# Optimization experiments

Measured on AMD Instinct MI355X. Metric: run time of the kernel, lower is better.

## Reference

```python
import jax, jax.numpy as jnp
import numpy as np

EPS = 1e-8


def setup_inputs() -> dict:
    key = jax.random.key(0)
    k1, k2 = jax.random.split(key)
    latent = jax.random.normal(k1, (16, 192, 64, 64), dtype=jnp.float32)
    codebook = jax.random.normal(k2, (1024, 192), dtype=jnp.float32)
    # codebook rows are unit-normalized at init in the original module
    codebook = codebook / jnp.linalg.norm(codebook, axis=-1, keepdims=True)
    return {"latent": latent, "codebook": codebook}


def reference(latent, codebook):
    b, c, h, w = latent.shape
    # [B,C,H,W] -> [N, C]
    x = jnp.transpose(latent, (0, 2, 3, 1)).reshape(-1, c)
    x = x / (jnp.linalg.norm(x, axis=-1, keepdims=True) + EPS)
    x2 = jnp.sum(x * x, axis=-1, keepdims=True)            # [N,1]
    c2 = jnp.sum(codebook * codebook, axis=-1)             # [K]
    dist_sq = x2 - 2.0 * jnp.einsum('nd,kd->nk', x, codebook) + c2[None, :]
    indices = jnp.argmin(dist_sq, axis=-1)                 # [N]
    quantized_flat = codebook[indices]                     # [N,C] gather
    quantized = jnp.transpose(quantized_flat.reshape(b, h, w, c), (0, 3, 1, 2))
    return quantized, indices.reshape(b, h, w)
```

## Files before the change

kernel.cpp:

```cpp
#include <hip/hip_runtime.h>


#define NPTS   65536
#define DIMS   192
#define KCB    1024
#define HW     4096
#define QELEMS 12582912

typedef __attribute__((ext_vector_type(8))) _Float16 f16x8;
typedef __attribute__((ext_vector_type(4))) _Float16 f16x4;
typedef __attribute__((ext_vector_type(4))) float f32x4;


__device__ __forceinline__ void async_load16(const void* g, void* l) {
    __builtin_amdgcn_global_load_lds(
        (const __attribute__((address_space(1))) unsigned int*)g,
        (__attribute__((address_space(3))) unsigned int*)l, 16, 0, 0);
}

__device__ __forceinline__ void top3_ins(unsigned& b, unsigned& s, unsigned& t,
                                         unsigned p) {
    unsigned m1 = min(b, p);
    unsigned m2 = min(s, p);
    b = max(b, p);
    s = max(s, m1);
    t = max(t, m2);
}

__global__ __launch_bounds__(256) void k_prep(const float* __restrict__ cbk,
                                              _Float16* __restrict__ Bpf,
                                              float* __restrict__ cbkT,
                                              float* __restrict__ c2) {
    __shared__ float q[16 * 193];
    const int tid = threadIdx.x;
    const int k0 = blockIdx.x * 16;
    const int lane = tid & 63;
    const int grp = tid >> 6;
    for (int r = grp; r < 16; r += 4) {
        const float* row = cbk + (size_t)(k0 + r) * DIMS;
        for (int c = lane; c < DIMS; c += 64) q[r * 193 + c] = row[c];
    }
    __syncthreads();
    {
        const int kl = tid & 15, dg = tid >> 4;
        for (int d = dg; d < DIMS; d += 16)
            cbkT[(size_t)d * KCB + k0 + kl] = q[kl * 193 + d];
    }
    for (int r = grp; r < 16; r += 4)
        for (int c = lane; c < DIMS; c += 64)
            Bpf[((size_t)(c >> 6) * KCB + k0 + r) * 64 + (c & 63)] =
                (_Float16)q[r * 193 + c];
    if (tid < 16) {
        float s = 0.f;
        #pragma unroll 4
        for (int c = 0; c < DIMS; ++c) {
            float v = q[tid * 193 + c];
            s = fmaf(v, v, s);
        }
        c2[k0 + tid] = s;
    }
}

__global__ __launch_bounds__(256, 2) void k_gemm_f(const float* __restrict__ latent,
                                                   const _Float16* __restrict__ Bpf,
                                                   const float* __restrict__ cbkT,
                                                   const float* __restrict__ c2,
                                                   const float* __restrict__ cbk,
                                                   float* __restrict__ out_q,
                                                   float* __restrict__ idxf) {
    __shared__ __align__(16) _Float16 As[128 * 200];
    __shared__ __align__(16) _Float16 Bs[2][4096];
    __shared__ float nrm_s[128];
    __shared__ uint4 t2buf[256];
    __shared__ int sidx[128];
    __shared__ int slist_pair[128];
    __shared__ int slist_full[128];
    __shared__ int scnt_pair, scnt_full;
    __shared__ float part8[8][32];
    __shared__ float inv8[8];
    __shared__ unsigned long long best8[8];

    const int tid = threadIdx.x;
    const int wave = tid >> 6;
    const int lane = tid & 63;
    const int quad = lane >> 4;
    const int l15 = lane & 15;
    const int wm = (wave >> 1) * 64;
    const int wn = (wave & 1) * 64;
    const int n0 = blockIdx.x * 128;
    const int bB = n0 >> 12;
    const int hw0 = n0 & 4095;
    const size_t latb = (size_t)bB * DIMS * HW;

    {
        float* part = (float*)&Bs[0][0];
        const float* lat = latent + latb + hw0;
        const int p = tid & 127, ch = tid >> 7;
        float ss = 0.f;
        #pragma unroll 4
        for (int i = 0; i < 24; ++i) {
            int c0 = i * 8 + ch * 4;
            float v0 = lat[(size_t)(c0 + 0) * HW + p];
            float v1 = lat[(size_t)(c0 + 1) * HW + p];
            float v2 = lat[(size_t)(c0 + 2) * HW + p];
            float v3 = lat[(size_t)(c0 + 3) * HW + p];
            ss = fmaf(v0, v0, fmaf(v1, v1, fmaf(v2, v2, fmaf(v3, v3, ss))));
            f16x4 h = { (_Float16)v0, (_Float16)v1, (_Float16)v2, (_Float16)v3 };
            *(f16x4*)&As[p * 200 + c0] = h;
        }
        part[ch * 128 + p] = ss;
        __syncthreads();
        if (tid < 128)
            nrm_s[tid] = sqrtf(part[tid] + part[128 + tid]);
        if (tid == 0) { scnt_pair = 0; scnt_full = 0; }
        __syncthreads();
    }

    const int sk0 = tid >> 2,        sj0 = (tid & 3) ^ ((sk0 >> 1) & 3);
    const int sk1 = (tid + 256) >> 2, sj1 = ((tid + 256) & 3) ^ ((sk1 >> 1) & 3);

    async_load16(Bpf + ((size_t)sk0) * 64 + sj0 * 8, &Bs[0][tid * 8]);
    async_load16(Bpf + ((size_t)sk1) * 64 + sj1 * 8, &Bs[0][(tid + 256) * 8]);

    unsigned rb[16], rs[16], rt[16];
    #pragma unroll
    for (int i = 0; i < 16; ++i) { rb[i] = 0u; rs[i] = 0u; rt[i] = 0u; }

    int nb_s = 0, h_s = 1;

    for (int nb = 0; nb < 8; ++nb) {
        f32x4 acc[4][4];
        #pragma unroll
        for (int mt = 0; mt < 4; ++mt)
            #pragma unroll
            for (int nt = 0; nt < 4; ++nt)
                #pragma unroll
                for (int r = 0; r < 4; ++r) acc[mt][nt][r] = 0.f;

        #pragma unroll
        for (int h = 0; h < 6; ++h) {
            const int ph = nb * 6 + h;
            asm volatile("s_waitcnt vmcnt(0)" ::: "memory");
            __syncthreads();
            if (ph < 47) {
                const size_t gb = ((size_t)(h_s >> 1) * KCB + nb_s * 128) * 64
                                  + (h_s & 1) * 32;
                async_load16(Bpf + gb + (size_t)sk0 * 64 + sj0 * 8,
                             &Bs[(ph + 1) & 1][tid * 8]);
                async_load16(Bpf + gb + (size_t)sk1 * 64 + sj1 * 8,
                             &Bs[(ph + 1) & 1][(tid + 256) * 8]);
                if (++h_s == 6) { h_s = 0; ++nb_s; }
            }
            const int g = h >> 1, s = h & 1;
            f16x8 af[4], bfr[4];
            #pragma unroll
            for (int mt = 0; mt < 4; ++mt) {
                int m = wm + mt * 16 + l15;
                af[mt] = *(const f16x8*)&As[m * 200 + g * 64 + s * 32 + quad * 8];
            }
            #pragma unroll
            for (int nt = 0; nt < 4; ++nt) {
                int n = wn + nt * 16 + l15;
                bfr[nt] = *(const f16x8*)&Bs[ph & 1][n * 32 + (quad ^ ((n >> 1) & 3)) * 8];
            }
            #pragma unroll
            for (int mt = 0; mt < 4; ++mt)
                #pragma unroll
                for (int nt = 0; nt < 4; ++nt)
                    acc[mt][nt] = __builtin_amdgcn_mfma_f32_16x16x32_f16(
                        af[mt], bfr[nt], acc[mt][nt], 0, 0, 0);
        }

        int kbase = nb * 128 + wn;
        #pragma unroll
        for (int mt = 0; mt < 4; ++mt) {
            #pragma unroll
            for (int r = 0; r < 4; ++r) {
                const int i = mt * 4 + r;
                #pragma unroll
                for (int nt = 0; nt < 4; ++nt) {
                    unsigned pv = ((unsigned)fmaf(acc[mt][nt][r], 65536.f, 2097152.f) << 10)
                                  | (unsigned)(kbase + nt * 16 + l15);
                    top3_ins(rb[i], rs[i], rt[i], pv);
                }
            }
        }
    }

    __syncthreads();
    #pragma unroll
    for (int i = 0; i < 16; ++i) {
        unsigned b = rb[i], s = rs[i], t = rt[i];
        #pragma unroll
        for (int off = 1; off < 16; off <<= 1) {
            unsigned ob = __shfl_xor(b, off, 64);
            unsigned os = __shfl_xor(s, off, 64);
            unsigned ot = __shfl_xor(t, off, 64);
            top3_ins(b, s, t, ob);
            top3_ins(b, s, t, os);
            top3_ins(b, s, t, ot);
        }
        if (l15 == 0) {
            int mt = i >> 2, r = i & 3;
            int mloc = wm + mt * 16 + quad * 4 + r;
            t2buf[mloc * 2 + (wave & 1)] = make_uint4(b, s, t, 0u);
        }
    }
    __syncthreads();
    if (tid < 128) {
        uint4 x = t2buf[tid * 2];
        uint4 y = t2buf[tid * 2 + 1];
        unsigned b = x.x, s = x.y, t = x.z;
        top3_ins(b, s, t, y.x);
        top3_ins(b, s, t, y.y);
        top3_ins(b, s, t, y.z);
        sidx[tid] = (int)(b & 1023u);
        unsigned q1 = b >> 10, q2 = s >> 10, q3 = t >> 10;
        unsigned Mq = (unsigned)fmaf(152.0f, nrm_s[tid], 4.0f);
        if (q1 - q3 < Mq) {
            int pos = atomicAdd(&scnt_full, 1);
            slist_full[pos] = tid;
        } else if (q1 - q2 < Mq) {
            int pos = atomicAdd(&scnt_pair, 1);
            slist_pair[pos] = tid | ((int)(b & 1023u) << 7)
                                  | ((int)(s & 1023u) << 17);
        }
    }
    __syncthreads();
    const int nfull = scnt_full;
    const int npair = scnt_pair;

    {
        float* xsf = (float*)As;
        const float4* ct = (const float4*)cbkT;
        const int j8 = tid >> 5, dl = tid & 31;
        for (int base = 0; base < nfull; base += 8) {
            const bool valid = (base + j8) < nfull;
            const int ploc = valid ? slist_full[base + j8] : 0;
            float ss = 0.f;
            if (valid) {
                #pragma unroll
                for (int i = 0; i < 6; ++i) {
                    int d = dl + i * 32;
                    float v = latent[latb + (size_t)d * HW + hw0 + ploc];
                    xsf[j8 * 200 + d] = v;
                    ss = fmaf(v, v, ss);
                }
            }
            part8[j8][dl] = ss;
            if (tid < 8) best8[tid] = ~0ull;
            __syncthreads();
            if (tid < 8) {
                float s = 0.f;
                #pragma unroll
                for (int i = 0; i < 32; ++i) s += part8[tid][i];
                inv8[tid] = 1.0f / (sqrtf(s) + 1e-8f);
            }
            __syncthreads();
            float4 a[8];
            #pragma unroll
            for (int p = 0; p < 8; ++p) a[p] = make_float4(0.f, 0.f, 0.f, 0.f);
            for (int d = 0; d < DIMS; d += 4) {
                float4 cv0 = ct[(size_t)(d + 0) * 256 + tid];
                float4 cv1 = ct[(size_t)(d + 1) * 256 + tid];
                float4 cv2 = ct[(size_t)(d + 2) * 256 + tid];
                float4 cv3 = ct[(size_t)(d + 3) * 256 + tid];
                #pragma unroll
                for (int p = 0; p < 8; ++p) {
                    float4 xv = *(const float4*)&xsf[p * 200 + d];
                    a[p].x = fmaf(xv.x, cv0.x, a[p].x); a[p].y = fmaf(xv.x, cv0.y, a[p].y);
                    a[p].z = fmaf(xv.x, cv0.z, a[p].z); a[p].w = fmaf(xv.x, cv0.w, a[p].w);
                    a[p].x = fmaf(xv.y, cv1.x, a[p].x); a[p].y = fmaf(xv.y, cv1.y, a[p].y);
                    a[p].z = fmaf(xv.y, cv1.z, a[p].z); a[p].w = fmaf(xv.y, cv1.w, a[p].w);
                    a[p].x = fmaf(xv.z, cv2.x, a[p].x); a[p].y = fmaf(xv.z, cv2.y, a[p].y);
                    a[p].z = fmaf(xv.z, cv2.z, a[p].z); a[p].w = fmaf(xv.z, cv2.w, a[p].w);
                    a[p].x = fmaf(xv.w, cv3.x, a[p].x); a[p].y = fmaf(xv.w, cv3.y, a[p].y);
                    a[p].z = fmaf(xv.w, cv3.z, a[p].z); a[p].w = fmaf(xv.w, cv3.w, a[p].w);
                }
            }
            #pragma unroll
            for (int p = 0; p < 8; ++p) {
                float inv = inv8[p];
                float dot4[4] = {a[p].x, a[p].y, a[p].z, a[p].w};
                unsigned long long loc = ~0ull;
                #pragma unroll
                for (int e = 0; e < 4; ++e) {
                    int k = 4 * tid + e;
                    float dist = c2[k] - 2.f * inv * dot4[e];
                    unsigned ub = __float_as_uint(dist);
                    ub ^= (ub >> 31) ? 0xFFFFFFFFu : 0x80000000u;
                    unsigned long long pk =
                        ((unsigned long long)ub << 32) | (unsigned)k;
                    loc = loc < pk ? loc : pk;
                }
                #pragma unroll
                for (int off = 1; off < 64; off <<= 1) {
                    unsigned long long o = __shfl_xor(loc, off, 64);
                    loc = loc < o ? loc : o;
                }
                if ((tid & 63) == 0) atomicMin(&best8[p], loc);
            }
            __syncthreads();
            if (valid && dl == 0)
                sidx[ploc] = (int)(best8[j8] & 0xFFFFFFFFull);
            __syncthreads();
        }
    }

    for (int i = tid; i < npair; i += 256) {
        int pk = slist_pair[i];
        int ploc = pk & 127;
        int k1 = (pk >> 7) & 1023;
        int k2 = (pk >> 17) & 1023;
        const float* xr = latent + latb + hw0 + ploc;
        const float* c1 = cbk + (size_t)k1 * DIMS;
        const float* c2r = cbk + (size_t)k2 * DIMS;
        float a1 = 0.f, a2 = 0.f;
        float pp[16];
        #pragma unroll
        for (int e = 0; e < 16; ++e) pp[e] = 0.f;
        for (int d0 = 0; d0 < DIMS; d0 += 16) {
            #pragma unroll
            for (int e = 0; e < 16; ++e) {
                int d = d0 + e;
                float xv = xr[(size_t)d * HW];
                a1 = fmaf(xv, c1[d], a1);
                a2 = fmaf(xv, c2r[d], a2);
                pp[e] = fmaf(xv, xv, pp[e]);
            }
        }
        float ss = 0.f;
        #pragma unroll
        for (int e = 0; e < 16; ++e) ss += pp[e];
        float inv = 1.0f / (sqrtf(ss) + 1e-8f);
        float d1 = c2[k1] - 2.f * inv * a1;
        float d2 = c2[k2] - 2.f * inv * a2;
        unsigned u1 = __float_as_uint(d1);
        u1 ^= (u1 >> 31) ? 0xFFFFFFFFu : 0x80000000u;
        unsigned u2 = __float_as_uint(d2);
        u2 ^= (u2 >> 31) ? 0xFFFFFFFFu : 0x80000000u;
        unsigned long long p1 = ((unsigned long long)u1 << 32) | (unsigned)k1;
        unsigned long long p2 = ((unsigned long long)u2 << 32) | (unsigned)k2;
        sidx[ploc] = (int)((p1 < p2 ? p1 : p2) & 1023ull);
    }
    __syncthreads();

    if (tid < 128) idxf[n0 + tid] = (float)sidx[tid];
    __syncthreads();

    float* q = (float*)As;
    for (int chk = 0; chk < 4; ++chk) {
        int p0 = chk * 32;
        for (int r = wave; r < 32; r += 4) {
            const float* row = cbk + (size_t)sidx[p0 + r] * DIMS;
            for (int c = lane; c < DIMS; c += 64) q[r * 193 + c] = row[c];
        }
        __syncthreads();
        float* ob = out_q + latb + hw0 + p0;
        #pragma unroll
        for (int i = 0; i < 24; ++i) {
            int u = i * 256 + tid;
            int c = u >> 5, p = u & 31;
            ob[(size_t)c * HW + p] = q[p * 193 + c];
        }
        __syncthreads();
    }
}

__global__ __launch_bounds__(256) void k_norms_fb(const float* __restrict__ latent,
                                                  float* __restrict__ inv_norm) {
    __shared__ float red[256];
    const int tid = threadIdx.x;
    const int n0 = blockIdx.x * 128;
    const int nl = tid & 127;
    const int half = tid >> 7;
    const int b = n0 >> 12;
    const int hw = (n0 & 4095) + nl;
    const float* base = latent + (size_t)b * DIMS * HW + hw;
    float ssq = 0.f;
    for (int c = half; c < DIMS; c += 2) {
        float v = base[(size_t)c * HW];
        ssq = fmaf(v, v, ssq);
    }
    red[tid] = ssq;
    __syncthreads();
    if (half == 0) {
        float s = red[tid] + red[tid + 128];
        inv_norm[n0 + nl] = 1.0f / (sqrtf(s) + 1e-8f);
    }
}

__global__ __launch_bounds__(256) void k_c2_fb(const float* __restrict__ cbk,
                                               float* __restrict__ c2) {
    int k = blockIdx.x * 256 + threadIdx.x;
    if (k >= KCB) return;
    const float4* row = (const float4*)(cbk + (size_t)k * DIMS);
    float s = 0.f;
    #pragma unroll
    for (int i = 0; i < DIMS / 4; ++i) {
        float4 v = row[i];
        s += v.x * v.x + v.y * v.y + v.z * v.z + v.w * v.w;
    }
    c2[k] = s;
}

#define LDX  132
__global__ __launch_bounds__(256) void k_dist_fb(const float* __restrict__ latent,
                                                 const float* __restrict__ cbk,
                                                 const float* __restrict__ inv_norm,
                                                 const float* __restrict__ c2,
                                                 int* __restrict__ idx_out,
                                                 float* __restrict__ idxf_out) {
    __shared__ __align__(16) float xsm[64 * LDX];
    __shared__ __align__(16) float csm[64 * LDX];
    __shared__ unsigned long long red[128];
    const int tid = threadIdx.x;
    const int n0 = blockIdx.x * 128;
    const int b = n0 >> 12;
    const int hw0 = n0 & 4095;
    const int kt = tid & 15;
    const int mt = tid >> 4;
    const float* lat_base = latent + (size_t)b * DIMS * HW + hw0;
    float inv[8];
    #pragma unroll
    for (int i = 0; i < 8; ++i) inv[i] = inv_norm[n0 + mt * 8 + i];
    float best[8];
    int bidx[8];
    #pragma unroll
    for (int i = 0; i < 8; ++i) { best[i] = 3.4e38f; bidx[i] = 0; }
    const int nl = tid & 127;
    const int cp = tid >> 7;
    for (int k0 = 0; k0 < KCB; k0 += 128) {
        float acc[8][8];
        #pragma unroll
        for (int i = 0; i < 8; ++i)
            #pragma unroll
            for (int j = 0; j < 8; ++j) acc[i][j] = 0.f;
        for (int d0 = 0; d0 < DIMS; d0 += 64) {
            __syncthreads();
            for (int cc = cp; cc < 64; cc += 2)
                xsm[cc * LDX + nl] = lat_base[(size_t)(d0 + cc) * HW + nl];
            #pragma unroll
            for (int i = 0; i < 8; ++i) {
                int f4 = tid + 256 * i;
                int kk = f4 >> 4;
                int dq = f4 & 15;
                float4 v = *(const float4*)(cbk + (size_t)(k0 + kk) * DIMS + d0 + dq * 4);
                csm[(dq * 4 + 0) * LDX + kk] = v.x;
                csm[(dq * 4 + 1) * LDX + kk] = v.y;
                csm[(dq * 4 + 2) * LDX + kk] = v.z;
                csm[(dq * 4 + 3) * LDX + kk] = v.w;
            }
            __syncthreads();
            for (int d = 0; d < 64; ++d) {
                const float* xr = &xsm[d * LDX + mt * 8];
                const float* cr = &csm[d * LDX + kt * 8];
                float x8[8], c8[8];
                *(float4*)&x8[0] = *(const float4*)&xr[0];
                *(float4*)&x8[4] = *(const float4*)&xr[4];
                *(float4*)&c8[0] = *(const float4*)&cr[0];
                *(float4*)&c8[4] = *(const float4*)&cr[4];
                #pragma unroll
                for (int i = 0; i < 8; ++i)
                    #pragma unroll
                    for (int j = 0; j < 8; ++j)
                        acc[i][j] = fmaf(x8[i], c8[j], acc[i][j]);
            }
        }
        float cc2[8];
        #pragma unroll
        for (int j = 0; j < 8; ++j) cc2[j] = c2[k0 + kt * 8 + j];
        #pragma unroll
        for (int i = 0; i < 8; ++i)
            #pragma unroll
            for (int j = 0; j < 8; ++j) {
                float t = inv[i] * acc[i][j];
                float dist = fmaf(-2.f, t, cc2[j]);
                int kidx = k0 + kt * 8 + j;
                if (dist < best[i]) { best[i] = dist; bidx[i] = kidx; }
            }
    }
    if (tid < 128) red[tid] = ~0ull;
    __syncthreads();
    #pragma unroll
    for (int i = 0; i < 8; ++i) {
        unsigned long long p =
            ((unsigned long long)__float_as_uint(best[i]) << 32) | (unsigned)bidx[i];
        atomicMin(&red[mt * 8 + i], p);
    }
    __syncthreads();
    if (tid < 128) {
        int k = (int)(red[tid] & 0xFFFFFFFFu);
        idx_out[n0 + tid] = k;
        idxf_out[n0 + tid] = (float)k;
    }
}

__global__ __launch_bounds__(256) void k_gather(const float* __restrict__ cbk,
                                                const int* __restrict__ idx,
                                                float* __restrict__ out) {
    __shared__ float q[64 * 193];
    __shared__ int sidx[64];
    const int tid = threadIdx.x;
    const int n0 = blockIdx.x * 64;
    const int b = n0 >> 12;
    const int hw0 = n0 & 4095;
    const int lane = tid & 63;
    const int grp = tid >> 6;

    if (tid < 64) sidx[tid] = idx[n0 + tid];
    __syncthreads();
    for (int r = grp; r < 64; r += 4) {
        const float* row = cbk + (size_t)sidx[r] * DIMS;
        for (int c = lane; c < DIMS; c += 64) q[r * 193 + c] = row[c];
    }
    __syncthreads();
    float* obase = out + (size_t)b * DIMS * HW + hw0;
    for (int c = grp; c < DIMS; c += 4) {
        obase[(size_t)c * HW + lane] = q[lane * 193 + c];
    }
}

extern "C" void kernel_launch(void* const* d_in, const int* in_sizes, int n_in,
                              void* d_out, int out_size, void* d_ws, size_t ws_size,
                              hipStream_t stream) {
    const float* latent = (const float*)d_in[0];
    const float* cbk = (const float*)d_in[1];
    float* out = (float*)d_out;
    float* out_q = out;
    float* out_idx = out + QELEMS;

    if (ws_size >= 2u * 1024u * 1024u) {
        char* w = (char*)d_ws;
        _Float16* Bpf = (_Float16*)w;
        float* cbkT = (float*)(w + 393216);
        float* c2 = (float*)(w + 1179648);

        k_prep<<<KCB / 16, 256, 0, stream>>>(cbk, Bpf, cbkT, c2);
        k_gemm_f<<<512, 256, 0, stream>>>(latent, Bpf, cbkT, c2, cbk,
                                          out_q, out_idx);
    } else {
        float* inv_norm = (float*)d_ws;
        float* c2 = inv_norm + NPTS;
        int* idx = (int*)(c2 + KCB);
        k_norms_fb<<<NPTS / 128, 256, 0, stream>>>(latent, inv_norm);
        k_c2_fb<<<4, 256, 0, stream>>>(cbk, c2);
        k_dist_fb<<<NPTS / 128, 256, 0, stream>>>(latent, cbk, inv_norm, c2, idx, out_idx);
        k_gather<<<NPTS / 64, 256, 0, stream>>>(cbk, idx, out_q);
    }
}
```

Baseline: 194.9 us.

## Triple-buffer codebook tiles with deeper async prefetch and overlay epilogue smem

Codebook B tiles go from double to triple buffering. The async loads are now issued two phases ahead, and each phase waits with vmcnt(2) instead of vmcnt(0), so global-to-LDS latency overlaps more of the MFMA work. The first two tiles are prefetched before the latent load and normalization, overlapping that setup with codebook fetches. To keep LDS usage, and so the 2-blocks-per-CU occupancy, roughly unchanged, the epilogue scratch arrays are overlaid onto a dead region of As. This depends on careful offsets and on correct barrier ordering.

```diff
diff --git a/kernel.cpp b/kernel.cpp
--- a/kernel.cpp
+++ b/kernel.cpp
@@ -69,16 +69,19 @@
                                                    float* __restrict__ out_q,
                                                    float* __restrict__ idxf) {
     __shared__ __align__(16) _Float16 As[128 * 200];
-    __shared__ __align__(16) _Float16 Bs[2][4096];
+    __shared__ __align__(16) _Float16 Bs[3][4096];
     __shared__ float nrm_s[128];
-    __shared__ uint4 t2buf[256];
-    __shared__ int sidx[128];
-    __shared__ int slist_pair[128];
-    __shared__ int slist_full[128];
-    __shared__ int scnt_pair, scnt_full;
-    __shared__ float part8[8][32];
-    __shared__ float inv8[8];
-    __shared__ unsigned long long best8[8];
+    __shared__ float part0[256];
+
+    char* ovl = (char*)As + 32768;
+    uint4* t2buf = (uint4*)ovl;
+    int* sidx = (int*)(ovl + 4096);
+    int* slist_pair = (int*)(ovl + 4608);
+    int* slist_full = (int*)(ovl + 5120);
+    int* scnts = (int*)(ovl + 5632);
+    float* part8 = (float*)(ovl + 5696);
+    float* inv8 = (float*)(ovl + 6720);
+    unsigned long long* best8 = (unsigned long long*)(ovl + 6784);
 
     const int tid = threadIdx.x;
     const int wave = tid >> 6;
@@ -92,8 +95,15 @@
     const int hw0 = n0 & 4095;
     const size_t latb = (size_t)bB * DIMS * HW;
 
+    const int sk0 = tid >> 2,         sj0 = (tid & 3) ^ ((sk0 >> 1) & 3);
+    const int sk1 = (tid + 256) >> 2, sj1 = ((tid + 256) & 3) ^ ((sk1 >> 1) & 3);
+
+    async_load16(Bpf + (size_t)sk0 * 64 + sj0 * 8, &Bs[0][tid * 8]);
+    async_load16(Bpf + (size_t)sk1 * 64 + sj1 * 8, &Bs[0][(tid + 256) * 8]);
+    async_load16(Bpf + (size_t)sk0 * 64 + sj0 * 8 + 32, &Bs[1][tid * 8]);
+    async_load16(Bpf + (size_t)sk1 * 64 + sj1 * 8 + 32, &Bs[1][(tid + 256) * 8]);
+
     {
-        float* part = (float*)&Bs[0][0];
         const float* lat = latent + latb + hw0;
         const int p = tid & 127, ch = tid >> 7;
         float ss = 0.f;
@@ -108,25 +118,19 @@
             f16x4 h = { (_Float16)v0, (_Float16)v1, (_Float16)v2, (_Float16)v3 };
             *(f16x4*)&As[p * 200 + c0] = h;
         }
-        part[ch * 128 + p] = ss;
+        part0[ch * 128 + p] = ss;
         __syncthreads();
         if (tid < 128)
-            nrm_s[tid] = sqrtf(part[tid] + part[128 + tid]);
-        if (tid == 0) { scnt_pair = 0; scnt_full = 0; }
+            nrm_s[tid] = sqrtf(part0[tid] + part0[128 + tid]);
         __syncthreads();
     }
-
-    const int sk0 = tid >> 2,        sj0 = (tid & 3) ^ ((sk0 >> 1) & 3);
-    const int sk1 = (tid + 256) >> 2, sj1 = ((tid + 256) & 3) ^ ((sk1 >> 1) & 3);
-
-    async_load16(Bpf + ((size_t)sk0) * 64 + sj0 * 8, &Bs[0][tid * 8]);
-    async_load16(Bpf + ((size_t)sk1) * 64 + sj1 * 8, &Bs[0][(tid + 256) * 8]);
 
     unsigned rb[16], rs[16], rt[16];
     #pragma unroll
     for (int i = 0; i < 16; ++i) { rb[i] = 0u; rs[i] = 0u; rt[i] = 0u; }
 
-    int nb_s = 0, h_s = 1;
+    int bc = 0;
+    int nb_s = 0, h_s = 2;
 
     for (int nb = 0; nb < 8; ++nb) {
         f32x4 acc[4][4];
@@ -139,16 +143,21 @@
 
         #pragma unroll
         for (int h = 0; h < 6; ++h) {
-            const int ph = nb * 6 + h;
-            asm volatile("s_waitcnt vmcnt(0)" ::: "memory");
-            __syncthreads();
-            if (ph < 47) {
+            if (nb == 7 && h == 5) {
+                asm volatile("s_waitcnt vmcnt(0)" ::: "memory");
+            } else {
+                asm volatile("s_waitcnt vmcnt(2)" ::: "memory");
+            }
+            __builtin_amdgcn_s_barrier();
+            asm volatile("" ::: "memory");
+            if (!(nb == 7 && h >= 4)) {
+                const int bt = (bc >= 1) ? bc - 1 : bc + 2;
                 const size_t gb = ((size_t)(h_s >> 1) * KCB + nb_s * 128) * 64
                                   + (h_s & 1) * 32;
                 async_load16(Bpf + gb + (size_t)sk0 * 64 + sj0 * 8,
-                             &Bs[(ph + 1) & 1][tid * 8]);
+                             &Bs[bt][tid * 8]);
                 async_load16(Bpf + gb + (size_t)sk1 * 64 + sj1 * 8,
-                             &Bs[(ph + 1) & 1][(tid + 256) * 8]);
+                             &Bs[bt][(tid + 256) * 8]);
                 if (++h_s == 6) { h_s = 0; ++nb_s; }
             }
             const int g = h >> 1, s = h & 1;
@@ -161,7 +170,7 @@
             #pragma unroll
             for (int nt = 0; nt < 4; ++nt) {
                 int n = wn + nt * 16 + l15;
-                bfr[nt] = *(const f16x8*)&Bs[ph & 1][n * 32 + (quad ^ ((n >> 1) & 3)) * 8];
+                bfr[nt] = *(const f16x8*)&Bs[bc][n * 32 + (quad ^ ((n >> 1) & 3)) * 8];
             }
             #pragma unroll
             for (int mt = 0; mt < 4; ++mt)
@@ -169,6 +178,7 @@
                 for (int nt = 0; nt < 4; ++nt)
                     acc[mt][nt] = __builtin_amdgcn_mfma_f32_16x16x32_f16(
                         af[mt], bfr[nt], acc[mt][nt], 0, 0, 0);
+            bc = (bc == 2) ? 0 : bc + 1;
         }
 
         int kbase = nb * 128 + wn;
@@ -188,6 +198,7 @@
     }
 
     __syncthreads();
+    if (tid == 0) { scnts[0] = 0; scnts[1] = 0; }
     #pragma unroll
     for (int i = 0; i < 16; ++i) {
         unsigned b = rb[i], s = rs[i], t = rt[i];
@@ -218,17 +229,17 @@
         unsigned q1 = b >> 10, q2 = s >> 10, q3 = t >> 10;
         unsigned Mq = (unsigned)fmaf(152.0f, nrm_s[tid], 4.0f);
         if (q1 - q3 < Mq) {
-            int pos = atomicAdd(&scnt_full, 1);
+            int pos = atomicAdd(&scnts[1], 1);
             slist_full[pos] = tid;
         } else if (q1 - q2 < Mq) {
-            int pos = atomicAdd(&scnt_pair, 1);
+            int pos = atomicAdd(&scnts[0], 1);
             slist_pair[pos] = tid | ((int)(b & 1023u) << 7)
                                   | ((int)(s & 1023u) << 17);
         }
     }
     __syncthreads();
-    const int nfull = scnt_full;
-    const int npair = scnt_pair;
+    const int nfull = scnts[1];
+    const int npair = scnts[0];
 
     {
         float* xsf = (float*)As;
@@ -247,13 +258,13 @@
                     ss = fmaf(v, v, ss);
                 }
             }
-            part8[j8][dl] = ss;
+            part8[j8 * 32 + dl] = ss;
             if (tid < 8) best8[tid] = ~0ull;
             __syncthreads();
             if (tid < 8) {
                 float s = 0.f;
                 #pragma unroll
-                for (int i = 0; i < 32; ++i) s += part8[tid][i];
+                for (int i = 0; i < 32; ++i) s += part8[tid * 32 + i];
                 inv8[tid] = 1.0f / (sqrtf(s) + 1e-8f);
             }
             __syncthreads();
```

Result: no change. 191.6 us (-1.7%).

## Halve points per block, overlay scratch LDS on B buffer, raise occupancy

Applied to the files above, without the earlier changes.

The fused GEMM/argmin kernel now handles 64 points per block instead of 128, launching 1024 blocks, and each wave computes 32 rows instead of 64. The post-GEMM scratch arrays (top-3 buffer, index lists, refinement buffers) are aliased onto the B double buffer, and the first B tile prefetch is issued before the latent load, shrinking LDS so launch bounds can request 3 blocks per CU. The aim is better latency hiding and an earlier start on the codebook fetch, at the cost of reloading the codebook tiles twice as often across blocks and doing less MFMA work per B fragment loaded.

```diff
diff --git a/kernel.cpp b/kernel.cpp
--- a/kernel.cpp
+++ b/kernel.cpp
@@ -61,45 +61,54 @@
     }
 }
 
-__global__ __launch_bounds__(256, 2) void k_gemm_f(const float* __restrict__ latent,
+__global__ __launch_bounds__(256, 3) void k_gemm_f(const float* __restrict__ latent,
                                                    const _Float16* __restrict__ Bpf,
                                                    const float* __restrict__ cbkT,
                                                    const float* __restrict__ c2,
                                                    const float* __restrict__ cbk,
                                                    float* __restrict__ out_q,
                                                    float* __restrict__ idxf) {
-    __shared__ __align__(16) _Float16 As[128 * 200];
+    __shared__ __align__(16) _Float16 As[64 * 200];
     __shared__ __align__(16) _Float16 Bs[2][4096];
-    __shared__ float nrm_s[128];
-    __shared__ uint4 t2buf[256];
-    __shared__ int sidx[128];
-    __shared__ int slist_pair[128];
-    __shared__ int slist_full[128];
-    __shared__ int scnt_pair, scnt_full;
-    __shared__ float part8[8][32];
-    __shared__ float inv8[8];
-    __shared__ unsigned long long best8[8];
+    __shared__ float nrm_s[64];
+    __shared__ float part0[256];
+
+    char* ovl = (char*)Bs;
+    uint4* t2buf = (uint4*)ovl;
+    int* sidx = (int*)(ovl + 2048);
+    int* slist_pair = (int*)(ovl + 2304);
+    int* slist_full = (int*)(ovl + 2560);
+    int* scnts = (int*)(ovl + 2816);
+    float* part8 = (float*)(ovl + 2824);
+    float* inv8 = (float*)(ovl + 3848);
+    unsigned long long* best8 = (unsigned long long*)(ovl + 3880);
+    float* xsf = (float*)(ovl + 8192);
 
     const int tid = threadIdx.x;
     const int wave = tid >> 6;
     const int lane = tid & 63;
     const int quad = lane >> 4;
     const int l15 = lane & 15;
-    const int wm = (wave >> 1) * 64;
+    const int wm = (wave >> 1) * 32;
     const int wn = (wave & 1) * 64;
-    const int n0 = blockIdx.x * 128;
+    const int n0 = blockIdx.x * 64;
     const int bB = n0 >> 12;
     const int hw0 = n0 & 4095;
     const size_t latb = (size_t)bB * DIMS * HW;
 
+    const int sk0 = tid >> 2,         sj0 = (tid & 3) ^ ((sk0 >> 1) & 3);
+    const int sk1 = (tid + 256) >> 2, sj1 = ((tid + 256) & 3) ^ ((sk1 >> 1) & 3);
+
+    async_load16(Bpf + (size_t)sk0 * 64 + sj0 * 8, &Bs[0][tid * 8]);
+    async_load16(Bpf + (size_t)sk1 * 64 + sj1 * 8, &Bs[0][(tid + 256) * 8]);
+
     {
-        float* part = (float*)&Bs[0][0];
         const float* lat = latent + latb + hw0;
-        const int p = tid & 127, ch = tid >> 7;
+        const int p = tid & 63, ch = tid >> 6;
         float ss = 0.f;
         #pragma unroll 4
-        for (int i = 0; i < 24; ++i) {
-            int c0 = i * 8 + ch * 4;
+        for (int i = 0; i < 12; ++i) {
+            int c0 = i * 16 + ch * 4;
             float v0 = lat[(size_t)(c0 + 0) * HW + p];
             float v1 = lat[(size_t)(c0 + 1) * HW + p];
             float v2 = lat[(size_t)(c0 + 2) * HW + p];
@@ -108,30 +117,24 @@
             f16x4 h = { (_Float16)v0, (_Float16)v1, (_Float16)v2, (_Float16)v3 };
             *(f16x4*)&As[p * 200 + c0] = h;
         }
-        part[ch * 128 + p] = ss;
+        part0[ch * 64 + p] = ss;
         __syncthreads();
-        if (tid < 128)
-            nrm_s[tid] = sqrtf(part[tid] + part[128 + tid]);
-        if (tid == 0) { scnt_pair = 0; scnt_full = 0; }
+        if (tid < 64)
+            nrm_s[tid] = sqrtf(part0[tid] + part0[64 + tid] +
+                               part0[128 + tid] + part0[192 + tid]);
         __syncthreads();
     }
 
-    const int sk0 = tid >> 2,        sj0 = (tid & 3) ^ ((sk0 >> 1) & 3);
-    const int sk1 = (tid + 256) >> 2, sj1 = ((tid + 256) & 3) ^ ((sk1 >> 1) & 3);
-
-    async_load16(Bpf + ((size_t)sk0) * 64 + sj0 * 8, &Bs[0][tid * 8]);
-    async_load16(Bpf + ((size_t)sk1) * 64 + sj1 * 8, &Bs[0][(tid + 256) * 8]);
-
-    unsigned rb[16], rs[16], rt[16];
+    unsigned rb[8], rs[8], rt[8];
     #pragma unroll
-    for (int i = 0; i < 16; ++i) { rb[i] = 0u; rs[i] = 0u; rt[i] = 0u; }
+    for (int i = 0; i < 8; ++i) { rb[i] = 0u; rs[i] = 0u; rt[i] = 0u; }
 
     int nb_s = 0, h_s = 1;
 
     for (int nb = 0; nb < 8; ++nb) {
-        f32x4 acc[4][4];
-        #pragma unroll
-        for (int mt = 0; mt < 4; ++mt)
+        f32x4 acc[2][4];
+        #pragma unroll
+        for (int mt = 0; mt < 2; ++mt)
             #pragma unroll
             for (int nt = 0; nt < 4; ++nt)
                 #pragma unroll
@@ -152,9 +155,9 @@
                 if (++h_s == 6) { h_s = 0; ++nb_s; }
             }
             const int g = h >> 1, s = h & 1;
-            f16x8 af[4], bfr[4];
-            #pragma unroll
-            for (int mt = 0; mt < 4; ++mt) {
+            f16x8 af[2], bfr[4];
+            #pragma unroll
+            for (int mt = 0; mt < 2; ++mt) {
                 int m = wm + mt * 16 + l15;
                 af[mt] = *(const f16x8*)&As[m * 200 + g * 64 + s * 32 + quad * 8];
             }
@@ -164,7 +167,7 @@
                 bfr[nt] = *(const f16x8*)&Bs[ph & 1][n * 32 + (quad ^ ((n >> 1) & 3)) * 8];
             }
             #pragma unroll
-            for (int mt = 0; mt < 4; ++mt)
+            for (int mt = 0; mt < 2; ++mt)
                 #pragma unroll
                 for (int nt = 0; nt < 4; ++nt)
                     acc[mt][nt] = __builtin_amdgcn_mfma_f32_16x16x32_f16(
@@ -173,7 +176,7 @@
 
         int kbase = nb * 128 + wn;
         #pragma unroll
-        for (int mt = 0; mt < 4; ++mt) {
+        for (int mt = 0; mt < 2; ++mt) {
             #pragma unroll
             for (int r = 0; r < 4; ++r) {
                 const int i = mt * 4 + r;
@@ -188,8 +191,9 @@
     }
 
     __syncthreads();
+    if (tid == 0) { scnts[0] = 0; scnts[1] = 0; }
     #pragma unroll
-    for (int i = 0; i < 16; ++i) {
+    for (int i = 0; i < 8; ++i) {
         unsigned b = rb[i], s = rs[i], t = rt[i];
         #pragma unroll
         for (int off = 1; off < 16; off <<= 1) {
@@ -207,7 +211,7 @@
         }
     }
     __syncthreads();
-    if (tid < 128) {
+    if (tid < 64) {
         uint4 x = t2buf[tid * 2];
         uint4 y = t2buf[tid * 2 + 1];
         unsigned b = x.x, s = x.y, t = x.z;
@@ -218,20 +222,19 @@
         unsigned q1 = b >> 10, q2 = s >> 10, q3 = t >> 10;
         unsigned Mq = (unsigned)fmaf(152.0f, nrm_s[tid], 4.0f);
         if (q1 - q3 < Mq) {
-            int pos = atomicAdd(&scnt_full, 1);
+            int pos = atomicAdd(&scnts[1], 1);
             slist_full[pos] = tid;
         } else if (q1 - q2 < Mq) {
-            int pos = atomicAdd(&scnt_pair, 1);
+            int pos = atomicAdd(&scnts[0], 1);
             slist_pair[pos] = tid | ((int)(b & 1023u) << 7)
                                   | ((int)(s & 1023u) << 17);
         }
     }
     __syncthreads();
-    const int nfull = scnt_full;
-    const int npair = scnt_pair;
+    const int nfull = scnts[1];
+    const int npair = scnts[0];
 
     {
-        float* xsf = (float*)As;
         const float4* ct = (const float4*)cbkT;
         const int j8 = tid >> 5, dl = tid & 31;
         for (int base = 0; base < nfull; base += 8) {
@@ -247,13 +250,13 @@
                     ss = fmaf(v, v, ss);
                 }
             }
-            part8[j8][dl] = ss;
+            part8[j8 * 32 + dl] = ss;
             if (tid < 8) best8[tid] = ~0ull;
             __syncthreads();
             if (tid < 8) {
                 float s = 0.f;
                 #pragma unroll
-                for (int i = 0; i < 32; ++i) s += part8[tid][i];
+                for (int i = 0; i < 32; ++i) s += part8[tid * 32 + i];
                 inv8[tid] = 1.0f / (sqrtf(s) + 1e-8f);
             }
             __syncthreads();
@@ -345,11 +348,11 @@
     }
     __syncthreads();
 
-    if (tid < 128) idxf[n0 + tid] = (float)sidx[tid];
+    if (tid < 64) idxf[n0 + tid] = (float)sidx[tid];
     __syncthreads();
 
     float* q = (float*)As;
-    for (int chk = 0; chk < 4; ++chk) {
+    for (int chk = 0; chk < 2; ++chk) {
         int p0 = chk * 32;
         for (int r = wave; r < 32; r += 4) {
             const float* row = cbk + (size_t)sidx[p0 + r] * DIMS;
@@ -537,8 +540,8 @@
         float* c2 = (float*)(w + 1179648);
 
         k_prep<<<KCB / 16, 256, 0, stream>>>(cbk, Bpf, cbkT, c2);
-        k_gemm_f<<<512, 256, 0, stream>>>(latent, Bpf, cbkT, c2, cbk,
-                                          out_q, out_idx);
+        k_gemm_f<<<NPTS / 64, 256, 0, stream>>>(latent, Bpf, cbkT, c2, cbk,
+                                                out_q, out_idx);
     } else {
         float* inv_norm = (float*)d_ws;
         float* c2 = inv_norm + NPTS;
```

After: 220.5 us. +13.1%, slower.
